# Kernel optimization log

Measured on AMD Instinct MI355X. Metric: run time of the kernel, lower is better.

The kernel has to match this reference:

```python
import jax, jax.numpy as jnp
import numpy as np

B, T, D, H = 8, 1024, 1024, 16
NSTEPS = 4  # num_recurrent_steps


def setup_inputs() -> dict:
    key = jax.random.key(0)
    ks = jax.random.split(key, 11)
    s = 0.02
    return {
        "x": jax.random.normal(ks[0], (B, T, D), jnp.float32),
        # nn.MultiheadAttention params (combined in_proj, out_proj)
        "in_proj_w": jax.random.normal(ks[1], (3 * D, D), jnp.float32) * s,
        "in_proj_b": jnp.zeros((3 * D,), jnp.float32),
        "out_proj_w": jax.random.normal(ks[2], (D, D), jnp.float32) * s,
        "out_proj_b": jnp.zeros((D,), jnp.float32),
        # nn.GRUCell params
        "w_ih": jax.random.normal(ks[3], (3 * D, D), jnp.float32) * s,
        "w_hh": jax.random.normal(ks[4], (3 * D, D), jnp.float32) * s,
        "b_ih": jnp.zeros((3 * D,), jnp.float32),
        "b_hh": jnp.zeros((3 * D,), jnp.float32),
        # gate Linear(2D -> D)
        "gate_w": jax.random.normal(ks[5], (D, 2 * D), jnp.float32) * s,
        "gate_b": jnp.zeros((D,), jnp.float32),
    }


def _mha(x, in_proj_w, in_proj_b, out_proj_w, out_proj_b):
    # PyTorch nn.MultiheadAttention math, batch_first, self-attention q=k=v=x.
    Bx, Tx, Dx = x.shape
    Dh = Dx // H
    qkv = x @ in_proj_w.T + in_proj_b          # [B,T,3D]
    q, k, v = jnp.split(qkv, 3, axis=-1)
    q = q.reshape(Bx, Tx, H, Dh)
    k = k.reshape(Bx, Tx, H, Dh)
    v = v.reshape(Bx, Tx, H, Dh)
    scores = jnp.einsum("bqhd,bkhd->bhqk", q, k) / jnp.sqrt(jnp.float32(Dh))
    attn = jax.nn.softmax(scores, axis=-1)     # [B,H,T,T]
    ctx = jnp.einsum("bhqk,bkhd->bqhd", attn, v).reshape(Bx, Tx, Dx)
    return ctx @ out_proj_w.T + out_proj_b     # [B,T,D]


def reference(x, in_proj_w, in_proj_b, out_proj_w, out_proj_b,
              w_ih, w_hh, b_ih, b_hh, gate_w, gate_b):
    Bx, Tx, Dx = x.shape
    # attention for each token is independent of the hidden state -> batch it
    attn_out = _mha(x, in_proj_w, in_proj_b, out_proj_w, out_proj_b)  # [B,T,D]

    def cell(h, xs):
        tok, a = xs  # each [B,D]
        for _ in range(NSTEPS):
            gi = tok @ w_ih.T + b_ih  # [B,3D]
            gh = h @ w_hh.T + b_hh    # [B,3D]
            ir, iz, inn = jnp.split(gi, 3, axis=-1)
            hr, hz, hn = jnp.split(gh, 3, axis=-1)
            r = jax.nn.sigmoid(ir + hr)
            z = jax.nn.sigmoid(iz + hz)
            n = jnp.tanh(inn + r * hn)
            h = (1.0 - z) * n + z * h
            g = jax.nn.sigmoid(jnp.concatenate([h, a], axis=-1) @ gate_w.T + gate_b)
            h = g * h + (1.0 - g) * a
        return h, h

    h0 = jnp.zeros((Bx, Dx), x.dtype)
    _, ys = jax.lax.scan(cell, h0, (x.transpose(1, 0, 2), attn_out.transpose(1, 0, 2)))
    return ys.transpose(1, 0, 2)  # [B,T,D]
```

## Files before the change

### kernel.cpp

```cpp
#include <hip/hip_runtime.h>
#include <hip/hip_bf16.h>
#include <math.h>
#include <stdint.h>

#define B 8
#define T 1024
#define D 1024
#define H 16
#define DH 64
#define NSTEPS 4

#define NCHAIN 4
#define ROWS_PER_CHAIN 2
#define NBLK_CHAIN 128
#define DIMS_PER_BLK 8

#define FLAG_STRIDE 16
#define RED_PITCH 37

__device__ __forceinline__ float sigmoidf_(float x) { return 1.0f / (1.0f + expf(-x)); }

__device__ __forceinline__ unsigned bf16rne(float f) {
    unsigned x = __float_as_uint(f);
    return (x + 0x7FFFu + ((x >> 16) & 1u)) >> 16;
}
#define UNPK(u, f0, f1)                                                       \
    { f0 = __uint_as_float((u) << 16); f1 = __uint_as_float((u) & 0xFFFF0000u); }

template <int MODE>
__global__ __launch_bounds__(256) void gemm_kernel(
    const float* __restrict__ A, const float* __restrict__ W,
    const float* __restrict__ bias, float* __restrict__ C,
    int M, int N, int K, int ldw, int koff,
    float* __restrict__ qb, float* __restrict__ kb, float* __restrict__ vb)
{
    __shared__ float As[32][68];
    __shared__ float Ws[32][68];
    const int m0 = blockIdx.x * 64, n0 = blockIdx.y * 64;
    const int tid = threadIdx.x;
    const int tn = tid & 15, tm = tid >> 4;
    float acc[4][4] = {};

    for (int k0 = 0; k0 < K; k0 += 32) {
#pragma unroll
        for (int j = 0; j < 2; ++j) {
            int lin = tid + j * 256;
            int r = lin >> 3, c4 = lin & 7;
            float4 av = *(const float4*)(A + (size_t)(m0 + r) * K + k0 + c4 * 4);
            As[c4 * 4 + 0][r] = av.x; As[c4 * 4 + 1][r] = av.y;
            As[c4 * 4 + 2][r] = av.z; As[c4 * 4 + 3][r] = av.w;
            float4 wv = *(const float4*)(W + (size_t)(n0 + r) * ldw + koff + k0 + c4 * 4);
            Ws[c4 * 4 + 0][r] = wv.x; Ws[c4 * 4 + 1][r] = wv.y;
            Ws[c4 * 4 + 2][r] = wv.z; Ws[c4 * 4 + 3][r] = wv.w;
        }
        __syncthreads();
#pragma unroll
        for (int k = 0; k < 32; ++k) {
            float a_[4], b_[4];
            *(float4*)a_ = *(const float4*)&As[k][tm * 4];
            *(float4*)b_ = *(const float4*)&Ws[k][tn * 4];
#pragma unroll
            for (int i = 0; i < 4; ++i)
#pragma unroll
                for (int j = 0; j < 4; ++j) acc[i][j] += a_[i] * b_[j];
        }
        __syncthreads();
    }

#pragma unroll
    for (int i = 0; i < 4; ++i) {
        int m = m0 + tm * 4 + i;
#pragma unroll
        for (int j = 0; j < 4; ++j) {
            int n = n0 + tn * 4 + j;
            float v = acc[i][j] + bias[n];
            if (MODE == 0) {
                C[(size_t)m * N + n] = v;
            } else {
                int which = n >> 10;
                int hh = (n & 1023) >> 6;
                int dh = n & 63;
                int b = m >> 10, t = m & 1023;
                float* dst = (which == 0) ? qb : ((which == 1) ? kb : vb);
                dst[(((size_t)(b * H + hh)) * T + t) * DH + dh] = v;
            }
        }
    }
}

__global__ __launch_bounds__(256) void attn_kernel(
    const float* __restrict__ qb, const float* __restrict__ kb,
    const float* __restrict__ vb, float* __restrict__ ctx)
{
    __shared__ float Qs[64][65];
    __shared__ float Ks[64][65];
    __shared__ float Vs[64][65];
    __shared__ float mrow[64], lrow[64], srow[64];
    __shared__ float tred[64][4];

    const int tid = threadIdx.x;
    const int row = tid & 63, seg = tid >> 6;
    const int bx = blockIdx.x;
    const int qblk = bx & 15;
    const int bh = bx >> 4;
    const float* qp = qb + (size_t)bh * T * DH;
    const float* kp = kb + (size_t)bh * T * DH;
    const float* vp = vb + (size_t)bh * T * DH;

#pragma unroll
    for (int i = 0; i < 4; ++i) {
        int lin = tid + i * 256;
        int r = lin >> 4, c4 = lin & 15;
        float4 v = *(const float4*)(qp + (size_t)(qblk * 64 + r) * DH + c4 * 4);
        Qs[r][c4 * 4 + 0] = v.x; Qs[r][c4 * 4 + 1] = v.y;
        Qs[r][c4 * 4 + 2] = v.z; Qs[r][c4 * 4 + 3] = v.w;
    }
    if (tid < 64) { mrow[tid] = -3.0e38f; lrow[tid] = 0.0f; }

    float Oacc[16];
#pragma unroll
    for (int j = 0; j < 16; ++j) Oacc[j] = 0.0f;

    for (int kt = 0; kt < 16; ++kt) {
        __syncthreads();
#pragma unroll
        for (int i = 0; i < 4; ++i) {
            int lin = tid + i * 256;
            int r = lin >> 4, c4 = lin & 15;
            float4 kv = *(const float4*)(kp + (size_t)(kt * 64 + r) * DH + c4 * 4);
            Ks[r][c4 * 4 + 0] = kv.x; Ks[r][c4 * 4 + 1] = kv.y;
            Ks[r][c4 * 4 + 2] = kv.z; Ks[r][c4 * 4 + 3] = kv.w;
            float4 vv = *(const float4*)(vp + (size_t)(kt * 64 + r) * DH + c4 * 4);
            Vs[r][c4 * 4 + 0] = vv.x; Vs[r][c4 * 4 + 1] = vv.y;
            Vs[r][c4 * 4 + 2] = vv.z; Vs[r][c4 * 4 + 3] = vv.w;
        }
        __syncthreads();

        float sacc[16];
#pragma unroll
        for (int j = 0; j < 16; ++j) sacc[j] = 0.0f;
        for (int k = 0; k < 64; ++k) {
            float qv = Qs[row][k];
#pragma unroll
            for (int j = 0; j < 16; ++j) sacc[j] += qv * Ks[seg * 16 + j][k];
        }
        float tmax = -3.0e38f;
#pragma unroll
        for (int j = 0; j < 16; ++j) { sacc[j] *= 0.125f; tmax = fmaxf(tmax, sacc[j]); }
        tred[row][seg] = tmax;
        __syncthreads();
        if (seg == 0) {
            float mt = fmaxf(fmaxf(tred[row][0], tred[row][1]),
                             fmaxf(tred[row][2], tred[row][3]));
            float mo = mrow[row];
            float mn = fmaxf(mo, mt);
            srow[row] = expf(mo - mn);
            mrow[row] = mn;
        }
        __syncthreads();
        float mn = mrow[row], sc = srow[row];
        float psum = 0.0f;
#pragma unroll
        for (int j = 0; j < 16; ++j) {
            float p = expf(sacc[j] - mn);
            Ks[row][seg * 16 + j] = p;
            psum += p;
        }
        tred[row][seg] = psum;
#pragma unroll
        for (int j = 0; j < 16; ++j) Oacc[j] *= sc;
        __syncthreads();
        if (seg == 0)
            lrow[row] = lrow[row] * sc +
                        (tred[row][0] + tred[row][1] + tred[row][2] + tred[row][3]);
        for (int kj = 0; kj < 64; ++kj) {
            float pv = Ks[row][kj];
#pragma unroll
            for (int j = 0; j < 16; ++j) Oacc[j] += pv * Vs[kj][seg * 16 + j];
        }
    }
    __syncthreads();
    float linv = 1.0f / lrow[row];
    int b = bh >> 4, hh = bh & 15;
    int q = qblk * 64 + row;
#pragma unroll
    for (int j = 0; j < 16; ++j)
        ctx[((size_t)(b * T + q)) * D + hh * 64 + seg * 16 + j] = Oacc[j] * linv;
}

__global__ __launch_bounds__(256, 1) void gru_persistent(
    const float* __restrict__ w_hh, const float* __restrict__ b_hh,
    const float* __restrict__ gate_w,
    const float* __restrict__ gi, const float* __restrict__ ga,
    const float* __restrict__ attn, float* __restrict__ out,
    float* __restrict__ hbuf, float* __restrict__ hpbuf,
    unsigned* __restrict__ flags)
{
    extern __shared__ float lds[];
    float* sh   = lds;
    float* redA = lds + 2048;

    const int tid = threadIdx.x;
    const int chain = blockIdx.x & 3;
    const int pos = blockIdx.x >> 2;
    const int d0 = pos * DIMS_PER_BLK;
    const int kp = tid & 31, jj = tid >> 5;
    const int d = d0 + jj;

    unsigned wpk[4][16];
#pragma unroll
    for (int tt = 0; tt < 4; ++tt) {
        const float* src = (tt < 3) ? (w_hh + ((size_t)(tt * D) + d) * D)
                                    : (gate_w + (size_t)d * (2 * D));
#pragma unroll
        for (int c = 0; c < 8; ++c) {
            float4 v = *(const float4*)(src + c * 128 + kp * 4);
            wpk[tt][c * 2]     = bf16rne(v.x) | (bf16rne(v.y) << 16);
            wpk[tt][c * 2 + 1] = bf16rne(v.z) | (bf16rne(v.w) << 16);
        }
    }

    float bfr = 0.0f, bfz = 0.0f, bfn = 0.0f;
    int fd = 0, fbg = 0;
    if (tid < 16) {
        int jj2 = tid >> 1, bl = tid & 1;
        fd = d0 + jj2;
        fbg = chain * ROWS_PER_CHAIN + bl;
        bfr = b_hh[fd]; bfz = b_hh[D + fd]; bfn = b_hh[2 * D + fd];
    }

    unsigned* flagbase = flags + (size_t)chain * NBLK_CHAIN * FLAG_STRIDE;
    const int srcA = tid >> 2;
    const int srcB = srcA + 64;
    const float* hsrc  = hbuf  + (size_t)chain * ROWS_PER_CHAIN * D;
    const float* hpsrc = hpbuf + (size_t)chain * ROWS_PER_CHAIN * D;

    unsigned bar = 0;
    float hpv = 0.0f;

#define POLL_AND_STAGE(SRC)                                                   \
    {                                                                         \
        const unsigned long long* p64_ = (const unsigned long long*)(SRC);    \
        while (__hip_atomic_load(flagbase + srcA * FLAG_STRIDE,               \
                   __ATOMIC_RELAXED, __HIP_MEMORY_SCOPE_AGENT) < bar) {}      \
        unsigned long long r0_ = __hip_atomic_load(p64_ + tid,                \
                __ATOMIC_RELAXED, __HIP_MEMORY_SCOPE_AGENT);                  \
        unsigned long long r2_ = __hip_atomic_load(p64_ + 512 + tid,          \
                __ATOMIC_RELAXED, __HIP_MEMORY_SCOPE_AGENT);                  \
        while (__hip_atomic_load(flagbase + srcB * FLAG_STRIDE,               \
                   __ATOMIC_RELAXED, __HIP_MEMORY_SCOPE_AGENT) < bar) {}      \
        unsigned long long r1_ = __hip_atomic_load(p64_ + 256 + tid,          \
                __ATOMIC_RELAXED, __HIP_MEMORY_SCOPE_AGENT);                  \
        unsigned long long r3_ = __hip_atomic_load(p64_ + 768 + tid,          \
                __ATOMIC_RELAXED, __HIP_MEMORY_SCOPE_AGENT);                  \
        unsigned long long* sh64_ = (unsigned long long*)sh;                  \
        sh64_[tid]       = r0_;                                               \
        sh64_[256 + tid] = r1_;                                               \
        sh64_[512 + tid] = r2_;                                               \
        sh64_[768 + tid] = r3_;                                               \
    }                                                                         \
    __syncthreads();

    for (int t = 0; t < T; ++t) {
        float giR = 0, giZ = 0, giN = 0, gav = 0, av = 0;
        if (tid < 16) {
            const size_t base = (size_t)fbg * T + t;
            const float* gib = gi + base * (3 * D);
            giR = gib[fd]; giZ = gib[D + fd]; giN = gib[2 * D + fd];
            gav = ga[base * D + fd];
            av  = attn[base * D + fd];
        }
        for (int s = 0; s < NSTEPS; ++s) {
            POLL_AND_STAGE(hsrc)
            float ho = 0.0f;
            if (tid < 16) ho = sh[(tid & 1) * 1024 + fd];
            {
                float ar[2] = {0, 0}, az[2] = {0, 0}, an[2] = {0, 0};
#pragma unroll
                for (int c = 0; c < 8; ++c) {
                    float wr0, wr1, wr2, wr3, wz0, wz1, wz2, wz3;
                    float wn0, wn1, wn2, wn3;
                    UNPK(wpk[0][c * 2],     wr0, wr1)
                    UNPK(wpk[0][c * 2 + 1], wr2, wr3)
                    UNPK(wpk[1][c * 2],     wz0, wz1)
                    UNPK(wpk[1][c * 2 + 1], wz2, wz3)
                    UNPK(wpk[2][c * 2],     wn0, wn1)
                    UNPK(wpk[2][c * 2 + 1], wn2, wn3)
                    const int ha = c * 128 + kp * 4;
#pragma unroll
                    for (int bl = 0; bl < 2; ++bl) {
                        float4 hv = *(const float4*)&sh[bl * 1024 + ha];
                        ar[bl] += hv.x * wr0 + hv.y * wr1 + hv.z * wr2 + hv.w * wr3;
                        az[bl] += hv.x * wz0 + hv.y * wz1 + hv.z * wz2 + hv.w * wz3;
                        an[bl] += hv.x * wn0 + hv.y * wn1 + hv.z * wn2 + hv.w * wn3;
                    }
                }
#pragma unroll
                for (int bl = 0; bl < 2; ++bl) {
                    redA[(jj * 6 + 0 + bl) * RED_PITCH + kp] = ar[bl];
                    redA[(jj * 6 + 2 + bl) * RED_PITCH + kp] = az[bl];
                    redA[(jj * 6 + 4 + bl) * RED_PITCH + kp] = an[bl];
                }
            }
            __syncthreads();
            if (tid < 16) {
                int base = (tid >> 1) * 6 + (tid & 1);
                float sr = 0, sz = 0, sn = 0;
#pragma unroll
                for (int c = 0; c < 8; ++c) {
                    float4 r4 = *(const float4*)&redA[(base    ) * RED_PITCH + c * 4];
                    float4 z4 = *(const float4*)&redA[(base + 2) * RED_PITCH + c * 4];
                    float4 n4 = *(const float4*)&redA[(base + 4) * RED_PITCH + c * 4];
                    sr += (r4.x + r4.y) + (r4.z + r4.w);
                    sz += (z4.x + z4.y) + (z4.z + z4.w);
                    sn += (n4.x + n4.y) + (n4.z + n4.w);
                }
                float r_ = sigmoidf_(giR + sr + bfr);
                float z_ = sigmoidf_(giZ + sz + bfz);
                float n_ = tanhf(giN + r_ * (sn + bfn));
                hpv = (1.0f - z_) * n_ + z_ * ho;
                __hip_atomic_store(hpbuf + (size_t)fbg * D + fd, hpv,
                                   __ATOMIC_RELAXED, __HIP_MEMORY_SCOPE_AGENT);
            }
            ++bar;
            if (tid < 64) {
                asm volatile("s_waitcnt vmcnt(0)" ::: "memory");
                if (tid == 0)
                    __hip_atomic_store(flagbase + pos * FLAG_STRIDE, bar,
                                       __ATOMIC_RELAXED, __HIP_MEMORY_SCOPE_AGENT);
            }

            POLL_AND_STAGE(hpsrc)
            {
                float ag[2] = {0, 0};
#pragma unroll
                for (int c = 0; c < 8; ++c) {
                    float wg0, wg1, wg2, wg3;
                    UNPK(wpk[3][c * 2],     wg0, wg1)
                    UNPK(wpk[3][c * 2 + 1], wg2, wg3)
                    const int ha = c * 128 + kp * 4;
#pragma unroll
                    for (int bl = 0; bl < 2; ++bl) {
                        float4 hv = *(const float4*)&sh[bl * 1024 + ha];
                        ag[bl] += hv.x * wg0 + hv.y * wg1 + hv.z * wg2 + hv.w * wg3;
                    }
                }
#pragma unroll
                for (int bl = 0; bl < 2; ++bl)
                    redA[(jj * 2 + bl) * RED_PITCH + kp] = ag[bl];
            }
            __syncthreads();
            float hn = 0.0f;
            if (tid < 16) {
                float sg = 0;
#pragma unroll
                for (int c = 0; c < 8; ++c) {
                    float4 v = *(const float4*)&redA[tid * RED_PITCH + c * 4];
                    sg += (v.x + v.y) + (v.z + v.w);
                }
                float g = sigmoidf_(sg + gav);
                hn = g * hpv + (1.0f - g) * av;
                __hip_atomic_store(hbuf + (size_t)fbg * D + fd, hn,
                                   __ATOMIC_RELAXED, __HIP_MEMORY_SCOPE_AGENT);
            }
            ++bar;
            if (tid < 64) {
                asm volatile("s_waitcnt vmcnt(0)" ::: "memory");
                if (tid == 0)
                    __hip_atomic_store(flagbase + pos * FLAG_STRIDE, bar,
                                       __ATOMIC_RELAXED, __HIP_MEMORY_SCOPE_AGENT);
            }
            if (tid < 16 && s == NSTEPS - 1)
                out[((size_t)fbg * T + t) * D + fd] = hn;
        }
    }
#undef POLL_AND_STAGE
}

extern "C" void kernel_launch(void* const* d_in, const int* in_sizes, int n_in,
                              void* d_out, int out_size, void* d_ws, size_t ws_size,
                              hipStream_t stream)
{
    const float* x          = (const float*)d_in[0];
    const float* in_proj_w  = (const float*)d_in[1];
    const float* in_proj_b  = (const float*)d_in[2];
    const float* out_proj_w = (const float*)d_in[3];
    const float* out_proj_b = (const float*)d_in[4];
    const float* w_ih       = (const float*)d_in[5];
    const float* w_hh       = (const float*)d_in[6];
    const float* b_ih       = (const float*)d_in[7];
    const float* b_hh       = (const float*)d_in[8];
    const float* gate_w     = (const float*)d_in[9];
    const float* gate_b     = (const float*)d_in[10];
    float* out = (float*)d_out;

    float* ws = (float*)d_ws;
    const size_t S1 = (size_t)B * H * T * DH;
    float* qb   = ws;
    float* kb   = ws + S1;
    float* vb   = ws + 2 * S1;
    float* ctx  = ws + 3 * S1;
    float* attn = ws + 4 * S1;
    float* ga   = ws + 5 * S1;
    float* gi   = ws;
    float* hbuf  = ws + 6 * S1;
    float* hpbuf = hbuf + B * D;
    unsigned* flags = (unsigned*)(hpbuf + B * D);

    dim3 blk(256);

    gemm_kernel<1><<<dim3(128, 48), blk, 0, stream>>>(
        x, in_proj_w, in_proj_b, nullptr, B * T, 3 * D, D, D, 0, qb, kb, vb);
    attn_kernel<<<dim3(2048), blk, 0, stream>>>(qb, kb, vb, ctx);
    gemm_kernel<0><<<dim3(128, 16), blk, 0, stream>>>(
        ctx, out_proj_w, out_proj_b, attn, B * T, D, D, D, 0,
        nullptr, nullptr, nullptr);
    gemm_kernel<0><<<dim3(128, 16), blk, 0, stream>>>(
        attn, gate_w, gate_b, ga, B * T, D, D, 2 * D, D,
        nullptr, nullptr, nullptr);
    gemm_kernel<0><<<dim3(128, 48), blk, 0, stream>>>(
        x, w_ih, b_ih, gi, B * T, 3 * D, D, D, 0,
        nullptr, nullptr, nullptr);

    hipMemsetAsync(hbuf, 0,
                   (2 * (size_t)B * D) * sizeof(float) +
                   NCHAIN * NBLK_CHAIN * FLAG_STRIDE * sizeof(unsigned),
                   stream);

    const int LDS_BYTES = 65536;
    static bool attr_done = false;
    if (!attr_done) {
        hipFuncSetAttribute((const void*)gru_persistent,
                            hipFuncAttributeMaxDynamicSharedMemorySize, LDS_BYTES);
        attr_done = true;
    }
    gru_persistent<<<dim3(NCHAIN * NBLK_CHAIN), blk, LDS_BYTES, stream>>>(
        w_hh, b_hh, gate_w, gi, ga, attn, out, hbuf, hpbuf, flags);
}
```

Measured before the change: 29.21 ms.

## Give each batch row its own GRU chain and use bf16 MFMA for input GEMMs

The persistent GRU kernel now runs 8 independent chains of 128 blocks, one per batch row, instead of 4 chains handling 2 rows each. Each block stages half as much hidden state and does half the dot-product work per step, and LDS per block drops so up to four blocks can share a CU. This is meant to shorten the serial per-step latency of the recurrence. The QKV projection and the w_ih projection move to a new bf16 MFMA GEMM with 128x128 tiles, which lowers precision on those products; the other two GEMMs keep the fp32 kernel.

```diff
diff --git a/kernel.cpp b/kernel.cpp
--- a/kernel.cpp
+++ b/kernel.cpp
@@ -10,13 +10,15 @@
 #define DH 64
 #define NSTEPS 4
 
-#define NCHAIN 4
-#define ROWS_PER_CHAIN 2
+#define NCHAIN 8
 #define NBLK_CHAIN 128
 #define DIMS_PER_BLK 8
 
 #define FLAG_STRIDE 16
 #define RED_PITCH 37
+
+typedef __attribute__((ext_vector_type(8))) short bhalf8;
+typedef __attribute__((ext_vector_type(4))) float f32x4;
 
 __device__ __forceinline__ float sigmoidf_(float x) { return 1.0f / (1.0f + expf(-x)); }
 
@@ -28,11 +30,107 @@
     { f0 = __uint_as_float((u) << 16); f1 = __uint_as_float((u) & 0xFFFF0000u); }
 
 template <int MODE>
-__global__ __launch_bounds__(256) void gemm_kernel(
+__global__ __launch_bounds__(256) void gemm_mfma(
     const float* __restrict__ A, const float* __restrict__ W,
     const float* __restrict__ bias, float* __restrict__ C,
     int M, int N, int K, int ldw, int koff,
     float* __restrict__ qb, float* __restrict__ kb, float* __restrict__ vb)
+{
+    __shared__ unsigned short Asm[128 * 32];
+    __shared__ unsigned short Wsm[128 * 32];
+    const int tid = threadIdx.x;
+    const int m0 = blockIdx.x * 128, n0 = blockIdx.y * 128;
+    const int lane = tid & 63, wave = tid >> 6;
+    const int wm = (wave >> 1) * 64, wn = (wave & 1) * 64;
+    const int sr = tid >> 1, sk = (tid & 1) * 16;
+
+    f32x4 acc[4][4] = {};
+
+    for (int k0 = 0; k0 < K; k0 += 32) {
+        {
+            const float* s = A + (size_t)(m0 + sr) * K + k0 + sk;
+            float4 a0 = *(const float4*)(s);
+            float4 a1 = *(const float4*)(s + 4);
+            float4 a2 = *(const float4*)(s + 8);
+            float4 a3 = *(const float4*)(s + 12);
+            uint4 p0, p1;
+            p0.x = bf16rne(a0.x) | (bf16rne(a0.y) << 16);
+            p0.y = bf16rne(a0.z) | (bf16rne(a0.w) << 16);
+            p0.z = bf16rne(a1.x) | (bf16rne(a1.y) << 16);
+            p0.w = bf16rne(a1.z) | (bf16rne(a1.w) << 16);
+            p1.x = bf16rne(a2.x) | (bf16rne(a2.y) << 16);
+            p1.y = bf16rne(a2.z) | (bf16rne(a2.w) << 16);
+            p1.z = bf16rne(a3.x) | (bf16rne(a3.y) << 16);
+            p1.w = bf16rne(a3.z) | (bf16rne(a3.w) << 16);
+            *(uint4*)&Asm[sr * 32 + sk]     = p0;
+            *(uint4*)&Asm[sr * 32 + sk + 8] = p1;
+        }
+        {
+            const float* s = W + (size_t)(n0 + sr) * ldw + koff + k0 + sk;
+            float4 a0 = *(const float4*)(s);
+            float4 a1 = *(const float4*)(s + 4);
+            float4 a2 = *(const float4*)(s + 8);
+            float4 a3 = *(const float4*)(s + 12);
+            uint4 p0, p1;
+            p0.x = bf16rne(a0.x) | (bf16rne(a0.y) << 16);
+            p0.y = bf16rne(a0.z) | (bf16rne(a0.w) << 16);
+            p0.z = bf16rne(a1.x) | (bf16rne(a1.y) << 16);
+            p0.w = bf16rne(a1.z) | (bf16rne(a1.w) << 16);
+            p1.x = bf16rne(a2.x) | (bf16rne(a2.y) << 16);
+            p1.y = bf16rne(a2.z) | (bf16rne(a2.w) << 16);
+            p1.z = bf16rne(a3.x) | (bf16rne(a3.y) << 16);
+            p1.w = bf16rne(a3.z) | (bf16rne(a3.w) << 16);
+            *(uint4*)&Wsm[sr * 32 + sk]     = p0;
+            *(uint4*)&Wsm[sr * 32 + sk + 8] = p1;
+        }
+        __syncthreads();
+
+        bhalf8 af[4], bf[4];
+#pragma unroll
+        for (int mi = 0; mi < 4; ++mi)
+            af[mi] = *(const bhalf8*)&Asm[(wm + mi * 16 + (lane & 15)) * 32 +
+                                          (lane >> 4) * 8];
+#pragma unroll
+        for (int ni = 0; ni < 4; ++ni)
+            bf[ni] = *(const bhalf8*)&Wsm[(wn + ni * 16 + (lane & 15)) * 32 +
+                                          (lane >> 4) * 8];
+#pragma unroll
+        for (int mi = 0; mi < 4; ++mi)
+#pragma unroll
+            for (int ni = 0; ni < 4; ++ni)
+                acc[mi][ni] = __builtin_amdgcn_mfma_f32_16x16x32_bf16(
+                    af[mi], bf[ni], acc[mi][ni], 0, 0, 0);
+        __syncthreads();
+    }
+
+#pragma unroll
+    for (int mi = 0; mi < 4; ++mi)
+#pragma unroll
+        for (int ni = 0; ni < 4; ++ni) {
+            int n = n0 + wn + ni * 16 + (lane & 15);
+            float bv = bias[n];
+#pragma unroll
+            for (int j = 0; j < 4; ++j) {
+                int m = m0 + wm + mi * 16 + (lane >> 4) * 4 + j;
+                float v = acc[mi][ni][j] + bv;
+                if (MODE == 0) {
+                    C[(size_t)m * N + n] = v;
+                } else {
+                    int which = n >> 10;
+                    int hh = (n & 1023) >> 6;
+                    int dh = n & 63;
+                    int b = m >> 10, t = m & 1023;
+                    float* dst = (which == 0) ? qb : ((which == 1) ? kb : vb);
+                    dst[(((size_t)(b * H + hh)) * T + t) * DH + dh] = v;
+                }
+            }
+        }
+}
+
+__global__ __launch_bounds__(256) void gemm_kernel(
+    const float* __restrict__ A, const float* __restrict__ W,
+    const float* __restrict__ bias, float* __restrict__ C,
+    int M, int N, int K, int ldw, int koff)
 {
     __shared__ float As[32][68];
     __shared__ float Ws[32][68];
@@ -73,17 +171,7 @@
 #pragma unroll
         for (int j = 0; j < 4; ++j) {
             int n = n0 + tn * 4 + j;
-            float v = acc[i][j] + bias[n];
-            if (MODE == 0) {
-                C[(size_t)m * N + n] = v;
-            } else {
-                int which = n >> 10;
-                int hh = (n & 1023) >> 6;
-                int dh = n & 63;
-                int b = m >> 10, t = m & 1023;
-                float* dst = (which == 0) ? qb : ((which == 1) ? kb : vb);
-                dst[(((size_t)(b * H + hh)) * T + t) * DH + dh] = v;
-            }
+            C[(size_t)m * N + n] = acc[i][j] + bias[n];
         }
     }
 }
@@ -188,7 +276,7 @@
         ctx[((size_t)(b * T + q)) * D + hh * 64 + seg * 16 + j] = Oacc[j] * linv;
 }
 
-__global__ __launch_bounds__(256, 1) void gru_persistent(
+__global__ __launch_bounds__(256, 4) void gru_persistent(
     const float* __restrict__ w_hh, const float* __restrict__ b_hh,
     const float* __restrict__ gate_w,
     const float* __restrict__ gi, const float* __restrict__ ga,
@@ -198,11 +286,11 @@
 {
     extern __shared__ float lds[];
     float* sh   = lds;
-    float* redA = lds + 2048;
+    float* redA = lds + 1024;
 
     const int tid = threadIdx.x;
-    const int chain = blockIdx.x & 3;
-    const int pos = blockIdx.x >> 2;
+    const int chain = blockIdx.x & 7;
+    const int pos = blockIdx.x >> 3;
     const int d0 = pos * DIMS_PER_BLK;
     const int kp = tid & 31, jj = tid >> 5;
     const int d = d0 + jj;
@@ -221,19 +309,17 @@
     }
 
     float bfr = 0.0f, bfz = 0.0f, bfn = 0.0f;
-    int fd = 0, fbg = 0;
-    if (tid < 16) {
-        int jj2 = tid >> 1, bl = tid & 1;
-        fd = d0 + jj2;
-        fbg = chain * ROWS_PER_CHAIN + bl;
+    int fd = 0;
+    if (tid < 8) {
+        fd = d0 + tid;
         bfr = b_hh[fd]; bfz = b_hh[D + fd]; bfn = b_hh[2 * D + fd];
     }
 
     unsigned* flagbase = flags + (size_t)chain * NBLK_CHAIN * FLAG_STRIDE;
     const int srcA = tid >> 2;
-    const int srcB = srcA + 64;
-    const float* hsrc  = hbuf  + (size_t)chain * ROWS_PER_CHAIN * D;
-    const float* hpsrc = hpbuf + (size_t)chain * ROWS_PER_CHAIN * D;
+    const int srcB = 64 + srcA;
+    const float* hsrc  = hbuf  + (size_t)chain * D;
+    const float* hpsrc = hpbuf + (size_t)chain * D;
 
     unsigned bar = 0;
     float hpv = 0.0f;
@@ -245,26 +331,20 @@
                    __ATOMIC_RELAXED, __HIP_MEMORY_SCOPE_AGENT) < bar) {}      \
         unsigned long long r0_ = __hip_atomic_load(p64_ + tid,                \
                 __ATOMIC_RELAXED, __HIP_MEMORY_SCOPE_AGENT);                  \
-        unsigned long long r2_ = __hip_atomic_load(p64_ + 512 + tid,          \
-                __ATOMIC_RELAXED, __HIP_MEMORY_SCOPE_AGENT);                  \
         while (__hip_atomic_load(flagbase + srcB * FLAG_STRIDE,               \
                    __ATOMIC_RELAXED, __HIP_MEMORY_SCOPE_AGENT) < bar) {}      \
         unsigned long long r1_ = __hip_atomic_load(p64_ + 256 + tid,          \
                 __ATOMIC_RELAXED, __HIP_MEMORY_SCOPE_AGENT);                  \
-        unsigned long long r3_ = __hip_atomic_load(p64_ + 768 + tid,          \
-                __ATOMIC_RELAXED, __HIP_MEMORY_SCOPE_AGENT);                  \
         unsigned long long* sh64_ = (unsigned long long*)sh;                  \
         sh64_[tid]       = r0_;                                               \
         sh64_[256 + tid] = r1_;                                               \
-        sh64_[512 + tid] = r2_;                                               \
-        sh64_[768 + tid] = r3_;                                               \
     }                                                                         \
     __syncthreads();
 
     for (int t = 0; t < T; ++t) {
         float giR = 0, giZ = 0, giN = 0, gav = 0, av = 0;
-        if (tid < 16) {
-            const size_t base = (size_t)fbg * T + t;
+        if (tid < 8) {
+            const size_t base = (size_t)chain * T + t;
             const float* gib = gi + base * (3 * D);
             giR = gib[fd]; giZ = gib[D + fd]; giN = gib[2 * D + fd];
             gav = ga[base * D + fd];
@@ -273,9 +353,9 @@
         for (int s = 0; s < NSTEPS; ++s) {
             POLL_AND_STAGE(hsrc)
             float ho = 0.0f;
-            if (tid < 16) ho = sh[(tid & 1) * 1024 + fd];
+            if (tid < 8) ho = sh[fd];
             {
-                float ar[2] = {0, 0}, az[2] = {0, 0}, an[2] = {0, 0};
+                float ar = 0, az = 0, an = 0;
 #pragma unroll
                 for (int c = 0; c < 8; ++c) {
                     float wr0, wr1, wr2, wr3, wz0, wz1, wz2, wz3;
@@ -286,31 +366,24 @@
                     UNPK(wpk[1][c * 2 + 1], wz2, wz3)
                     UNPK(wpk[2][c * 2],     wn0, wn1)
                     UNPK(wpk[2][c * 2 + 1], wn2, wn3)
-                    const int ha = c * 128 + kp * 4;
-#pragma unroll
-                    for (int bl = 0; bl < 2; ++bl) {
-                        float4 hv = *(const float4*)&sh[bl * 1024 + ha];
-                        ar[bl] += hv.x * wr0 + hv.y * wr1 + hv.z * wr2 + hv.w * wr3;
-                        az[bl] += hv.x * wz0 + hv.y * wz1 + hv.z * wz2 + hv.w * wz3;
-                        an[bl] += hv.x * wn0 + hv.y * wn1 + hv.z * wn2 + hv.w * wn3;
-                    }
+                    float4 hv = *(const float4*)&sh[c * 128 + kp * 4];
+                    ar += hv.x * wr0 + hv.y * wr1 + hv.z * wr2 + hv.w * wr3;
+                    az += hv.x * wz0 + hv.y * wz1 + hv.z * wz2 + hv.w * wz3;
+                    an += hv.x * wn0 + hv.y * wn1 + hv.z * wn2 + hv.w * wn3;
                 }
-#pragma unroll
-                for (int bl = 0; bl < 2; ++bl) {
-                    redA[(jj * 6 + 0 + bl) * RED_PITCH + kp] = ar[bl];
-                    redA[(jj * 6 + 2 + bl) * RED_PITCH + kp] = az[bl];
-                    redA[(jj * 6 + 4 + bl) * RED_PITCH + kp] = an[bl];
-                }
+                redA[(jj * 3 + 0) * RED_PITCH + kp] = ar;
+                redA[(jj * 3 + 1) * RED_PITCH + kp] = az;
+                redA[(jj * 3 + 2) * RED_PITCH + kp] = an;
             }
             __syncthreads();
-            if (tid < 16) {
-                int base = (tid >> 1) * 6 + (tid & 1);
+            if (tid < 8) {
+                int base = tid * 3;
                 float sr = 0, sz = 0, sn = 0;
 #pragma unroll
                 for (int c = 0; c < 8; ++c) {
                     float4 r4 = *(const float4*)&redA[(base    ) * RED_PITCH + c * 4];
-                    float4 z4 = *(const float4*)&redA[(base + 2) * RED_PITCH + c * 4];
-                    float4 n4 = *(const float4*)&redA[(base + 4) * RED_PITCH + c * 4];
+                    float4 z4 = *(const float4*)&redA[(base + 1) * RED_PITCH + c * 4];
+                    float4 n4 = *(const float4*)&redA[(base + 2) * RED_PITCH + c * 4];
                     sr += (r4.x + r4.y) + (r4.z + r4.w);
                     sz += (z4.x + z4.y) + (z4.z + z4.w);
                     sn += (n4.x + n4.y) + (n4.z + n4.w);
@@ -319,7 +392,7 @@
                 float z_ = sigmoidf_(giZ + sz + bfz);
                 float n_ = tanhf(giN + r_ * (sn + bfn));
                 hpv = (1.0f - z_) * n_ + z_ * ho;
-                __hip_atomic_store(hpbuf + (size_t)fbg * D + fd, hpv,
+                __hip_atomic_store(hpbuf + (size_t)chain * D + fd, hpv,
                                    __ATOMIC_RELAXED, __HIP_MEMORY_SCOPE_AGENT);
             }
             ++bar;
@@ -332,26 +405,20 @@
 
             POLL_AND_STAGE(hpsrc)
             {
-                float ag[2] = {0, 0};
+                float ag = 0;
 #pragma unroll
                 for (int c = 0; c < 8; ++c) {
                     float wg0, wg1, wg2, wg3;
                     UNPK(wpk[3][c * 2],     wg0, wg1)
                     UNPK(wpk[3][c * 2 + 1], wg2, wg3)
-                    const int ha = c * 128 + kp * 4;
-#pragma unroll
-                    for (int bl = 0; bl < 2; ++bl) {
-                        float4 hv = *(const float4*)&sh[bl * 1024 + ha];
-                        ag[bl] += hv.x * wg0 + hv.y * wg1 + hv.z * wg2 + hv.w * wg3;
-                    }
+                    float4 hv = *(const float4*)&sh[c * 128 + kp * 4];
+                    ag += hv.x * wg0 + hv.y * wg1 + hv.z * wg2 + hv.w * wg3;
                 }
-#pragma unroll
-                for (int bl = 0; bl < 2; ++bl)
-                    redA[(jj * 2 + bl) * RED_PITCH + kp] = ag[bl];
+                redA[jj * RED_PITCH + kp] = ag;
             }
             __syncthreads();
             float hn = 0.0f;
-            if (tid < 16) {
+            if (tid < 8) {
                 float sg = 0;
 #pragma unroll
                 for (int c = 0; c < 8; ++c) {
@@ -360,7 +427,7 @@
                 }
                 float g = sigmoidf_(sg + gav);
                 hn = g * hpv + (1.0f - g) * av;
-                __hip_atomic_store(hbuf + (size_t)fbg * D + fd, hn,
+                __hip_atomic_store(hbuf + (size_t)chain * D + fd, hn,
                                    __ATOMIC_RELAXED, __HIP_MEMORY_SCOPE_AGENT);
             }
             ++bar;
@@ -370,8 +437,8 @@
                     __hip_atomic_store(flagbase + pos * FLAG_STRIDE, bar,
                                        __ATOMIC_RELAXED, __HIP_MEMORY_SCOPE_AGENT);
             }
-            if (tid < 16 && s == NSTEPS - 1)
-                out[((size_t)fbg * T + t) * D + fd] = hn;
+            if (tid < 8 && s == NSTEPS - 1)
+                out[((size_t)chain * T + t) * D + fd] = hn;
         }
     }
 #undef POLL_AND_STAGE
@@ -409,31 +476,23 @@
 
     dim3 blk(256);
 
-    gemm_kernel<1><<<dim3(128, 48), blk, 0, stream>>>(
+    gemm_mfma<1><<<dim3(64, 24), blk, 0, stream>>>(
         x, in_proj_w, in_proj_b, nullptr, B * T, 3 * D, D, D, 0, qb, kb, vb);
     attn_kernel<<<dim3(2048), blk, 0, stream>>>(qb, kb, vb, ctx);
-    gemm_kernel<0><<<dim3(128, 16), blk, 0, stream>>>(
-        ctx, out_proj_w, out_proj_b, attn, B * T, D, D, D, 0,
-        nullptr, nullptr, nullptr);
-    gemm_kernel<0><<<dim3(128, 16), blk, 0, stream>>>(
-        attn, gate_w, gate_b, ga, B * T, D, D, 2 * D, D,
-        nullptr, nullptr, nullptr);
-    gemm_kernel<0><<<dim3(128, 48), blk, 0, stream>>>(
+    gemm_kernel<<<dim3(128, 16), blk, 0, stream>>>(
+        ctx, out_proj_w, out_proj_b, attn, B * T, D, D, D, 0);
+    gemm_kernel<<<dim3(128, 16), blk, 0, stream>>>(
+        attn, gate_w, gate_b, ga, B * T, D, D, 2 * D, D);
+    gemm_mfma<0><<<dim3(64, 24), blk, 0, stream>>>(
         x, w_ih, b_ih, gi, B * T, 3 * D, D, D, 0,
         nullptr, nullptr, nullptr);
 
     hipMemsetAsync(hbuf, 0,
                    (2 * (size_t)B * D) * sizeof(float) +
-                   NCHAIN * NBLK_CHAIN * FLAG_STRIDE * sizeof(unsigned),
+                   (size_t)NCHAIN * NBLK_CHAIN * FLAG_STRIDE * sizeof(unsigned),
                    stream);
 
-    const int LDS_BYTES = 65536;
-    static bool attr_done = false;
-    if (!attr_done) {
-        hipFuncSetAttribute((const void*)gru_persistent,
-                            hipFuncAttributeMaxDynamicSharedMemorySize, LDS_BYTES);
-        attr_done = true;
-    }
+    const int LDS_BYTES = 8192;
     gru_persistent<<<dim3(NCHAIN * NBLK_CHAIN), blk, LDS_BYTES, stream>>>(
         w_hh, b_hh, gate_w, gi, ga, attn, out, hbuf, hpbuf, flags);
 }
```

Result: slower. 105.3 ms (+260.6%).

## Replace FP32 SIMT GEMMs with bf16 MFMA 128x128-tile GEMM kernel

Applied to the files above, without the earlier changes.

The four dense projection GEMMs move from a scalar FP32 64x64 tiled kernel to a bf16 MFMA kernel with 128x128 block tiles. Operands are rounded to bf16 while being staged into shared memory, and each wave computes a 64x64 sub-tile using 16x16x32 bf16 matrix instructions. The aim is to cut the FP32 FMA cost of the pre-recurrence GEMMs. In exchange, the inputs lose precision to bf16, and the total time is likely dominated by the persistent GRU kernel, which is unchanged.

```diff
diff --git a/kernel.cpp b/kernel.cpp
--- a/kernel.cpp
+++ b/kernel.cpp
@@ -18,6 +18,9 @@
 #define FLAG_STRIDE 16
 #define RED_PITCH 37
 
+typedef __attribute__((ext_vector_type(8))) short bhalf8;
+typedef __attribute__((ext_vector_type(4))) float f32x4;
+
 __device__ __forceinline__ float sigmoidf_(float x) { return 1.0f / (1.0f + expf(-x)); }
 
 __device__ __forceinline__ unsigned bf16rne(float f) {
@@ -28,64 +31,101 @@
     { f0 = __uint_as_float((u) << 16); f1 = __uint_as_float((u) & 0xFFFF0000u); }
 
 template <int MODE>
-__global__ __launch_bounds__(256) void gemm_kernel(
+__global__ __launch_bounds__(256) void gemm_mfma(
     const float* __restrict__ A, const float* __restrict__ W,
     const float* __restrict__ bias, float* __restrict__ C,
     int M, int N, int K, int ldw, int koff,
     float* __restrict__ qb, float* __restrict__ kb, float* __restrict__ vb)
 {
-    __shared__ float As[32][68];
-    __shared__ float Ws[32][68];
-    const int m0 = blockIdx.x * 64, n0 = blockIdx.y * 64;
+    __shared__ unsigned short Asm[128 * 32];
+    __shared__ unsigned short Wsm[128 * 32];
     const int tid = threadIdx.x;
-    const int tn = tid & 15, tm = tid >> 4;
-    float acc[4][4] = {};
+    const int m0 = blockIdx.x * 128, n0 = blockIdx.y * 128;
+    const int lane = tid & 63, wave = tid >> 6;
+    const int wm = (wave >> 1) * 64, wn = (wave & 1) * 64;
+    const int sr = tid >> 1, sk = (tid & 1) * 16;
+
+    f32x4 acc[4][4] = {};
 
     for (int k0 = 0; k0 < K; k0 += 32) {
-#pragma unroll
-        for (int j = 0; j < 2; ++j) {
-            int lin = tid + j * 256;
-            int r = lin >> 3, c4 = lin & 7;
-            float4 av = *(const float4*)(A + (size_t)(m0 + r) * K + k0 + c4 * 4);
-            As[c4 * 4 + 0][r] = av.x; As[c4 * 4 + 1][r] = av.y;
-            As[c4 * 4 + 2][r] = av.z; As[c4 * 4 + 3][r] = av.w;
-            float4 wv = *(const float4*)(W + (size_t)(n0 + r) * ldw + koff + k0 + c4 * 4);
-            Ws[c4 * 4 + 0][r] = wv.x; Ws[c4 * 4 + 1][r] = wv.y;
-            Ws[c4 * 4 + 2][r] = wv.z; Ws[c4 * 4 + 3][r] = wv.w;
-        }
-        __syncthreads();
-#pragma unroll
-        for (int k = 0; k < 32; ++k) {
-            float a_[4], b_[4];
-            *(float4*)a_ = *(const float4*)&As[k][tm * 4];
-            *(float4*)b_ = *(const float4*)&Ws[k][tn * 4];
-#pragma unroll
-            for (int i = 0; i < 4; ++i)
-#pragma unroll
-                for (int j = 0; j < 4; ++j) acc[i][j] += a_[i] * b_[j];
-        }
-        __syncthreads();
-    }
-
-#pragma unroll
-    for (int i = 0; i < 4; ++i) {
-        int m = m0 + tm * 4 + i;
-#pragma unroll
-        for (int j = 0; j < 4; ++j) {
-            int n = n0 + tn * 4 + j;
-            float v = acc[i][j] + bias[n];
-            if (MODE == 0) {
-                C[(size_t)m * N + n] = v;
-            } else {
-                int which = n >> 10;
-                int hh = (n & 1023) >> 6;
-                int dh = n & 63;
-                int b = m >> 10, t = m & 1023;
-                float* dst = (which == 0) ? qb : ((which == 1) ? kb : vb);
-                dst[(((size_t)(b * H + hh)) * T + t) * DH + dh] = v;
-            }
-        }
-    }
+        {
+            const float* s = A + (size_t)(m0 + sr) * K + k0 + sk;
+            float4 a0 = *(const float4*)(s);
+            float4 a1 = *(const float4*)(s + 4);
+            float4 a2 = *(const float4*)(s + 8);
+            float4 a3 = *(const float4*)(s + 12);
+            uint4 p0, p1;
+            p0.x = bf16rne(a0.x) | (bf16rne(a0.y) << 16);
+            p0.y = bf16rne(a0.z) | (bf16rne(a0.w) << 16);
+            p0.z = bf16rne(a1.x) | (bf16rne(a1.y) << 16);
+            p0.w = bf16rne(a1.z) | (bf16rne(a1.w) << 16);
+            p1.x = bf16rne(a2.x) | (bf16rne(a2.y) << 16);
+            p1.y = bf16rne(a2.z) | (bf16rne(a2.w) << 16);
+            p1.z = bf16rne(a3.x) | (bf16rne(a3.y) << 16);
+            p1.w = bf16rne(a3.z) | (bf16rne(a3.w) << 16);
+            *(uint4*)&Asm[sr * 32 + sk]     = p0;
+            *(uint4*)&Asm[sr * 32 + sk + 8] = p1;
+        }
+        {
+            const float* s = W + (size_t)(n0 + sr) * ldw + koff + k0 + sk;
+            float4 a0 = *(const float4*)(s);
+            float4 a1 = *(const float4*)(s + 4);
+            float4 a2 = *(const float4*)(s + 8);
+            float4 a3 = *(const float4*)(s + 12);
+            uint4 p0, p1;
+            p0.x = bf16rne(a0.x) | (bf16rne(a0.y) << 16);
+            p0.y = bf16rne(a0.z) | (bf16rne(a0.w) << 16);
+            p0.z = bf16rne(a1.x) | (bf16rne(a1.y) << 16);
+            p0.w = bf16rne(a1.z) | (bf16rne(a1.w) << 16);
+            p1.x = bf16rne(a2.x) | (bf16rne(a2.y) << 16);
+            p1.y = bf16rne(a2.z) | (bf16rne(a2.w) << 16);
+            p1.z = bf16rne(a3.x) | (bf16rne(a3.y) << 16);
+            p1.w = bf16rne(a3.z) | (bf16rne(a3.w) << 16);
+            *(uint4*)&Wsm[sr * 32 + sk]     = p0;
+            *(uint4*)&Wsm[sr * 32 + sk + 8] = p1;
+        }
+        __syncthreads();
+
+        bhalf8 af[4], bf[4];
+#pragma unroll
+        for (int mi = 0; mi < 4; ++mi)
+            af[mi] = *(const bhalf8*)&Asm[(wm + mi * 16 + (lane & 15)) * 32 +
+                                          (lane >> 4) * 8];
+#pragma unroll
+        for (int ni = 0; ni < 4; ++ni)
+            bf[ni] = *(const bhalf8*)&Wsm[(wn + ni * 16 + (lane & 15)) * 32 +
+                                          (lane >> 4) * 8];
+#pragma unroll
+        for (int mi = 0; mi < 4; ++mi)
+#pragma unroll
+            for (int ni = 0; ni < 4; ++ni)
+                acc[mi][ni] = __builtin_amdgcn_mfma_f32_16x16x32_bf16(
+                    af[mi], bf[ni], acc[mi][ni], 0, 0, 0);
+        __syncthreads();
+    }
+
+#pragma unroll
+    for (int mi = 0; mi < 4; ++mi)
+#pragma unroll
+        for (int ni = 0; ni < 4; ++ni) {
+            int n = n0 + wn + ni * 16 + (lane & 15);
+            float bv = bias[n];
+#pragma unroll
+            for (int j = 0; j < 4; ++j) {
+                int m = m0 + wm + mi * 16 + (lane >> 4) * 4 + j;
+                float v = acc[mi][ni][j] + bv;
+                if (MODE == 0) {
+                    C[(size_t)m * N + n] = v;
+                } else {
+                    int which = n >> 10;
+                    int hh = (n & 1023) >> 6;
+                    int dh = n & 63;
+                    int b = m >> 10, t = m & 1023;
+                    float* dst = (which == 0) ? qb : ((which == 1) ? kb : vb);
+                    dst[(((size_t)(b * H + hh)) * T + t) * DH + dh] = v;
+                }
+            }
+        }
 }
 
 __global__ __launch_bounds__(256) void attn_kernel(
@@ -409,22 +449,22 @@
 
     dim3 blk(256);
 
-    gemm_kernel<1><<<dim3(128, 48), blk, 0, stream>>>(
+    gemm_mfma<1><<<dim3(64, 24), blk, 0, stream>>>(
         x, in_proj_w, in_proj_b, nullptr, B * T, 3 * D, D, D, 0, qb, kb, vb);
     attn_kernel<<<dim3(2048), blk, 0, stream>>>(qb, kb, vb, ctx);
-    gemm_kernel<0><<<dim3(128, 16), blk, 0, stream>>>(
+    gemm_mfma<0><<<dim3(64, 8), blk, 0, stream>>>(
         ctx, out_proj_w, out_proj_b, attn, B * T, D, D, D, 0,
         nullptr, nullptr, nullptr);
-    gemm_kernel<0><<<dim3(128, 16), blk, 0, stream>>>(
+    gemm_mfma<0><<<dim3(64, 8), blk, 0, stream>>>(
         attn, gate_w, gate_b, ga, B * T, D, D, 2 * D, D,
         nullptr, nullptr, nullptr);
-    gemm_kernel<0><<<dim3(128, 48), blk, 0, stream>>>(
+    gemm_mfma<0><<<dim3(64, 24), blk, 0, stream>>>(
         x, w_ih, b_ih, gi, B * T, 3 * D, D, D, 0,
         nullptr, nullptr, nullptr);
 
     hipMemsetAsync(hbuf, 0,
                    (2 * (size_t)B * D) * sizeof(float) +
-                   NCHAIN * NBLK_CHAIN * FLAG_STRIDE * sizeof(unsigned),
+                   (size_t)NCHAIN * NBLK_CHAIN * FLAG_STRIDE * sizeof(unsigned),
                    stream);
 
     const int LDS_BYTES = 65536;
```

After: 27.09 ms, median of 2. -7.3%, faster.
